# Kernel tuning notes

Hardware: AMD Instinct MI355X
Metric: run time of the kernel (lower is better)

## Reference

```python
import jax, jax.numpy as jnp
import numpy as np

N, E, C_IN, C_OUT, G = 100000, 1250000, 64, 64, 64
H = 2 * C_OUT  # hidden width of conv1 output


def _lin(k, out_d, in_d, scale=0.05):
    kw, kb = jax.random.split(k)
    return (jax.random.normal(kw, (out_d, in_d), jnp.float32) * scale,
            jax.random.normal(kb, (out_d,), jnp.float32) * scale)


def setup_inputs() -> dict:
    key = jax.random.key(0)
    ks = jax.random.split(key, 12)
    x = jax.random.normal(ks[0], (N, C_IN), jnp.float32)
    edge_index = jax.random.randint(ks[1], (2, E), 0, N, jnp.int64)
    batch = jnp.sort(jax.random.randint(ks[2], (N,), 0, G, jnp.int64))
    # GraphConv layer 1: lin_rel (with bias) on aggregated msgs, lin_root (no bias) on x
    w1_rel, b1_rel = _lin(ks[3], H, C_IN)
    w1_root = jax.random.normal(ks[4], (H, C_IN), jnp.float32) * 0.05
    # GraphConv layer 2
    w2_rel, b2_rel = _lin(ks[5], C_OUT, H)
    w2_root = jax.random.normal(ks[6], (C_OUT, H), jnp.float32) * 0.05
    # encoder_S: out_channels -> 8 -> 4 -> 1
    es_w1, es_b1 = _lin(ks[7], 8, C_OUT)
    es_w2, es_b2 = _lin(ks[8], 4, 8)
    es_w3, es_b3 = _lin(ks[9], 1, 4)
    # decoder: 1 -> 4 -> 8 -> out_channels (input dim fixed from buggy 2 to 1)
    d_w1, d_b1 = _lin(ks[10], 4, 1)
    d_w2, d_b2 = _lin(ks[11], 8, 4)
    d_w3, d_b3 = _lin(jax.random.fold_in(key, 99), C_OUT, 8)
    return dict(x=x, edge_index=edge_index, batch=batch,
                w1_rel=w1_rel, b1_rel=b1_rel, w1_root=w1_root,
                w2_rel=w2_rel, b2_rel=b2_rel, w2_root=w2_root,
                es_w1=es_w1, es_b1=es_b1, es_w2=es_w2, es_b2=es_b2,
                es_w3=es_w3, es_b3=es_b3,
                d_w1=d_w1, d_b1=d_b1, d_w2=d_w2, d_b2=d_b2,
                d_w3=d_w3, d_b3=d_b3)


def reference(x, edge_index, batch,
              w1_rel, b1_rel, w1_root,
              w2_rel, b2_rel, w2_root,
              es_w1, es_b1, es_w2, es_b2, es_w3, es_b3,
              d_w1, d_b1, d_w2, d_b2, d_w3, d_b3):
    src, dst = edge_index[0], edge_index[1]
    # GraphConv 1: sum-aggregate source feats into targets, then rel+root linears
    agg1 = jax.ops.segment_sum(x[src], dst, num_segments=N)  # [N, C_IN]
    h1 = jax.nn.relu(agg1 @ w1_rel.T + b1_rel + x @ w1_root.T)  # [N, H]
    # GraphConv 2
    agg2 = jax.ops.segment_sum(h1[src], dst, num_segments=N)
    h2 = jax.nn.relu(agg2 @ w2_rel.T + b2_rel + h1 @ w2_root.T)  # [N, C_OUT]
    # global mean pool over graphs
    counts = jax.ops.segment_sum(jnp.ones((N,), h2.dtype), batch, num_segments=G)
    h3 = jax.ops.segment_sum(h2, batch, num_segments=G) / jnp.maximum(counts, 1.0)[:, None]  # [G, C_OUT]
    # encoder_S MLP -> z
    z = jax.nn.relu(h3 @ es_w1.T + es_b1)
    z = jax.nn.relu(z @ es_w2.T + es_b2)
    z = z @ es_w3.T + es_b3  # [G, 1]
    # decoder MLP -> x_
    x_ = jax.nn.relu(z @ d_w1.T + d_b1)
    x_ = jax.nn.relu(x_ @ d_w2.T + d_b2)
    x_ = x_ @ d_w3.T + d_b3  # [G, C_OUT]
    return h3, x_
```

## Files before the change

### kernel.cpp

```cpp
#include <hip/hip_runtime.h>
#include <stdint.h>

#define NN 100000
#define EE 1250000
#define NBUCK 196
#define CHUNK 4096
#define NCHUNK ((EE + CHUNK - 1) / CHUNK)
#define PSLICE 24
#define XB_NB ((NN * 64 / 4 + 255) / 256)

typedef __attribute__((ext_vector_type(8))) short short8;
typedef __attribute__((ext_vector_type(4))) float f32x4;

__device__ inline ushort f2bf(float f) {
  union { float f; uint32_t u; } v; v.f = f;
  uint32_t r = v.u + 0x7FFF + ((v.u >> 16) & 1);
  return (ushort)(r >> 16);
}
__device__ inline float bf2f(ushort h) {
  union { uint32_t u; float f; } v; v.u = ((uint32_t)h) << 16;
  return v.f;
}

__global__ __launch_bounds__(256) void kfront(const float* __restrict__ w1_rel,
                                              const float* __restrict__ w1_root,
                                              const float* __restrict__ w2_rel,
                                              const float* __restrict__ w2_root,
                                              const float* __restrict__ x,
                                              const int* __restrict__ dstI,
                                              ushort* __restrict__ WF,
                                              ushort* __restrict__ xb,
                                              int* __restrict__ histG) {
  __shared__ int h[NBUCK];
  int t = threadIdx.x;
  int blk = blockIdx.x;
  if (blk < 32) {
    int idx = blk * 256 + t;
    if (idx < 8192) {
      int j = idx & 7, l = (idx >> 3) & 63, ts = idx >> 9;
      {
        int s = ts & 1, tt = ts >> 1;
        int o = tt * 16 + (l & 15), k = s * 32 + (l >> 4) * 8 + j;
        WF[idx] = f2bf(w1_rel[o * 64 + k]);
        WF[8192 + idx] = f2bf(w1_root[o * 64 + k]);
      }
      {
        int s = ts & 3, tt = ts >> 2;
        int o = tt * 16 + (l & 15), k = s * 32 + (l >> 4) * 8 + j;
        WF[16384 + idx] = f2bf(w2_rel[o * 128 + k]);
        WF[24576 + idx] = f2bf(w2_root[o * 128 + k]);
      }
    }
  } else if (blk < 32 + XB_NB) {
    int i = ((blk - 32) * 256 + t) * 4;
    if (i < NN * 64) {
      float4 v = *reinterpret_cast<const float4*>(x + i);
      ushort o[4] = {f2bf(v.x), f2bf(v.y), f2bf(v.z), f2bf(v.w)};
      *reinterpret_cast<uint2*>(xb + i) = *reinterpret_cast<uint2*>(o);
    }
  } else {
    int c = blk - 32 - XB_NB;
    if (t < NBUCK) h[t] = 0;
    __syncthreads();
    int cb = c * CHUNK;
    int cc = EE - cb; if (cc > CHUNK) cc = CHUNK;
    for (int i = t; i < cc; i += 256) atomicAdd(&h[dstI[cb + i] >> 9], 1);
    __syncthreads();
    if (t < NBUCK) histG[c * NBUCK + t] = h[t];
  }
}

__global__ __launch_bounds__(512) void kscan2d(const int* __restrict__ histG,
                                               int* __restrict__ relG,
                                               int* __restrict__ bucketTotal) {
  __shared__ int sm[512];
  int b = blockIdx.x;
  int t = threadIdx.x;
  int v = (t < NCHUNK) ? histG[t * NBUCK + b] : 0;
  sm[t] = v;
  __syncthreads();
  for (int d = 1; d < 512; d <<= 1) {
    int u = (t >= d) ? sm[t - d] : 0;
    __syncthreads();
    sm[t] += u;
    __syncthreads();
  }
  if (t < NCHUNK) relG[t * NBUCK + b] = sm[t] - v;
  if (t == 511) bucketTotal[b] = sm[511];
}

__global__ __launch_bounds__(256) void kbinA2(const int* __restrict__ srcI,
                                              const int* __restrict__ dstI,
                                              const int* __restrict__ histG,
                                              const int* __restrict__ relG,
                                              const int* __restrict__ bucketTotal,
                                              uint32_t* __restrict__ pairsG) {
  __shared__ uint32_t pko[CHUNK];
  __shared__ int ss[256];
  __shared__ int bsL[NBUCK];
  __shared__ int ex[NBUCK + 1];
  __shared__ int cur[NBUCK];
  __shared__ int gb[NBUCK];
  int t = threadIdx.x;
  int cb = blockIdx.x * CHUNK;
  int cc = EE - cb; if (cc > CHUNK) cc = CHUNK;

  {
    int bv = (t < NBUCK) ? bucketTotal[t] : 0;
    ss[t] = bv;
    __syncthreads();
    for (int d = 1; d < 256; d <<= 1) {
      int u = (t >= d) ? ss[t - d] : 0;
      __syncthreads();
      ss[t] += u;
      __syncthreads();
    }
    if (t < NBUCK) bsL[t] = ss[t] - bv;
    __syncthreads();
  }
  int v = (t < NBUCK) ? histG[blockIdx.x * NBUCK + t] : 0;
  ss[t] = v;
  __syncthreads();
  for (int d = 1; d < 256; d <<= 1) {
    int u = (t >= d) ? ss[t - d] : 0;
    __syncthreads();
    ss[t] += u;
    __syncthreads();
  }
  if (t < NBUCK) {
    ex[t] = ss[t] - v;
    cur[t] = ss[t] - v;
    gb[t] = bsL[t] + relG[blockIdx.x * NBUCK + t];
  }
  if (t == NBUCK - 1) ex[NBUCK] = ss[t];
  __syncthreads();
  for (int i = t; i < cc; i += 256) {
    int d = dstI[cb + i];
    int s = srcI[cb + i];
    int b = d >> 9;
    int p = atomicAdd(&cur[b], 1);
    pko[p] = (uint32_t)s | ((uint32_t)(d & 511) << 17);
  }
  __syncthreads();
  if (t < NBUCK) {
    int base = ex[t], cnt = ex[t + 1] - base, g0 = gb[t];
    for (int j = 0; j < cnt; ++j) pairsG[g0 + j] = pko[base + j];
  }
}

__global__ __launch_bounds__(256) void kbinB(const uint32_t* __restrict__ pairsG,
                                             const int* __restrict__ bucketTotal,
                                             int* __restrict__ starts,
                                             int* __restrict__ esrc) {
  __shared__ int hist[512];
  __shared__ int ex2[512];
  __shared__ int part[256];
  __shared__ int baseS;
  int t = threadIdx.x;
  int b = blockIdx.x;
  int nbase = b << 9;
  {
    int bv = (t < NBUCK) ? bucketTotal[t] : 0;
    part[t] = bv;
    __syncthreads();
    for (int d = 1; d < 256; d <<= 1) {
      int u = (t >= d) ? part[t - d] : 0;
      __syncthreads();
      part[t] += u;
      __syncthreads();
    }
    if (t == b) baseS = part[t] - bv;
    __syncthreads();
  }
  int base = baseS;
  int ecnt = bucketTotal[b];

  hist[t] = 0; hist[t + 256] = 0;
  __syncthreads();
  for (int i = t; i < ecnt; i += 256) atomicAdd(&hist[pairsG[base + i] >> 17], 1);
  __syncthreads();
  int a = hist[2 * t], c = hist[2 * t + 1];
  part[t] = a + c;
  __syncthreads();
  for (int d = 1; d < 256; d <<= 1) {
    int u = (t >= d) ? part[t - d] : 0;
    __syncthreads();
    part[t] += u;
    __syncthreads();
  }
  int pex = part[t] - (a + c);
  ex2[2 * t] = pex;
  ex2[2 * t + 1] = pex + a;
  __syncthreads();
  for (int n = t; n < 512; n += 256) {
    int node = nbase + n;
    if (node < NN) starts[node] = base + ex2[n];
  }
  if (b == NBUCK - 1 && t == 0) starts[NN] = EE;
  for (int n = t; n < 512; n += 256) hist[n] = ex2[n];
  __syncthreads();
  for (int i = t; i < ecnt; i += 256) {
    uint32_t p = pairsG[base + i];
    int dl = p >> 17;
    int s = p & 0x1FFFF;
    int lp = atomicAdd(&hist[dl], 1);
    esrc[base + lp] = s;
  }
}

#define ACC8(u)                                                                    \
  a0 += bf2f((ushort)(u).x); a1 += bf2f((ushort)((u).x >> 16));                    \
  a2 += bf2f((ushort)(u).y); a3 += bf2f((ushort)((u).y >> 16));                    \
  a4 += bf2f((ushort)(u).z); a5 += bf2f((ushort)((u).z >> 16));                    \
  a6 += bf2f((ushort)(u).w); a7 += bf2f((ushort)((u).w >> 16));

#define GATHER_CORE8(featb)                                                        \
  float a0 = 0.f, a1 = 0.f, a2 = 0.f, a3 = 0.f,                                    \
        a4 = 0.f, a5 = 0.f, a6 = 0.f, a7 = 0.f;                                    \
  const ushort* fb = (featb) + 8 * lg;                                             \
  int i = b;                                                                       \
  {                                                                                \
    int s0 = 0, s1 = 0, s2 = 0, s3 = 0, s4 = 0, s5 = 0, s6 = 0, s7 = 0;            \
    bool have = (i + 8 <= e);                                                      \
    if (have) {                                                                    \
      s0 = esrc[i];     s1 = esrc[i + 1]; s2 = esrc[i + 2]; s3 = esrc[i + 3];      \
      s4 = esrc[i + 4]; s5 = esrc[i + 5]; s6 = esrc[i + 6]; s7 = esrc[i + 7];      \
    }                                                                              \
    while (have) {                                                                 \
      uint4 u0 = *(const uint4*)(fb + (size_t)s0 * 64);                            \
      uint4 u1 = *(const uint4*)(fb + (size_t)s1 * 64);                            \
      uint4 u2 = *(const uint4*)(fb + (size_t)s2 * 64);                            \
      uint4 u3 = *(const uint4*)(fb + (size_t)s3 * 64);                            \
      uint4 u4 = *(const uint4*)(fb + (size_t)s4 * 64);                            \
      uint4 u5 = *(const uint4*)(fb + (size_t)s5 * 64);                            \
      uint4 u6 = *(const uint4*)(fb + (size_t)s6 * 64);                            \
      uint4 u7 = *(const uint4*)(fb + (size_t)s7 * 64);                            \
      i += 8;                                                                      \
      have = (i + 8 <= e);                                                         \
      if (have) {                                                                  \
        s0 = esrc[i];     s1 = esrc[i + 1]; s2 = esrc[i + 2]; s3 = esrc[i + 3];    \
        s4 = esrc[i + 4]; s5 = esrc[i + 5]; s6 = esrc[i + 6]; s7 = esrc[i + 7];    \
      }                                                                            \
      ACC8(u0) ACC8(u1) ACC8(u2) ACC8(u3) ACC8(u4) ACC8(u5) ACC8(u6) ACC8(u7)      \
    }                                                                              \
  }                                                                                \
  if (i + 4 <= e) {                                                                \
    int s0 = esrc[i], s1 = esrc[i + 1], s2 = esrc[i + 2], s3 = esrc[i + 3];        \
    uint4 u0 = *(const uint4*)(fb + (size_t)s0 * 64);                              \
    uint4 u1 = *(const uint4*)(fb + (size_t)s1 * 64);                              \
    uint4 u2 = *(const uint4*)(fb + (size_t)s2 * 64);                              \
    uint4 u3 = *(const uint4*)(fb + (size_t)s3 * 64);                              \
    ACC8(u0) ACC8(u1) ACC8(u2) ACC8(u3)                                            \
    i += 4;                                                                        \
  }                                                                                \
  if (i + 2 <= e) {                                                                \
    int s0 = esrc[i], s1 = esrc[i + 1];                                            \
    uint4 u0 = *(const uint4*)(fb + (size_t)s0 * 64);                              \
    uint4 u1 = *(const uint4*)(fb + (size_t)s1 * 64);                              \
    ACC8(u0) ACC8(u1)                                                              \
    i += 2;                                                                        \
  }                                                                                \
  if (i < e) {                                                                     \
    int s0 = esrc[i];                                                              \
    uint4 u0 = *(const uint4*)(fb + (size_t)s0 * 64);                              \
    ACC8(u0)                                                                       \
  }

__global__ __launch_bounds__(256) void kgatherQ(const ushort* __restrict__ featb,
                                                const int* __restrict__ starts,
                                                const int* __restrict__ esrc,
                                                ushort* __restrict__ outb) {
  int w = (blockIdx.x * 256 + threadIdx.x) >> 3;
  if (w >= NN) return;
  int lg = threadIdx.x & 7;
  int b = starts[w], e = starts[w + 1];
  GATHER_CORE8(featb)
  uint4 o;
  o.x = (uint32_t)f2bf(a0) | ((uint32_t)f2bf(a1) << 16);
  o.y = (uint32_t)f2bf(a2) | ((uint32_t)f2bf(a3) << 16);
  o.z = (uint32_t)f2bf(a4) | ((uint32_t)f2bf(a5) << 16);
  o.w = (uint32_t)f2bf(a6) | ((uint32_t)f2bf(a7) << 16);
  *(uint4*)(outb + (size_t)w * 64 + 8 * lg) = o;
}

__global__ __launch_bounds__(256) void kgh2Q(const ushort* __restrict__ featb,
                                             const int* __restrict__ starts,
                                             const int* __restrict__ esrc,
                                             const ushort* __restrict__ r2b,
                                             const float* __restrict__ b2v,
                                             ushort* __restrict__ h2b) {
  int w = (blockIdx.x * 256 + threadIdx.x) >> 3;
  if (w >= NN) return;
  int lg = threadIdx.x & 7;
  int b = starts[w], e = starts[w + 1];
  GATHER_CORE8(featb)
  uint4 ru = *(const uint4*)(r2b + (size_t)w * 64 + 8 * lg);
  float4 bA = *(const float4*)(b2v + 8 * lg);
  float4 bB = *(const float4*)(b2v + 8 * lg + 4);
  float v0 = fmaxf(a0 + bf2f((ushort)ru.x) + bA.x, 0.f);
  float v1 = fmaxf(a1 + bf2f((ushort)(ru.x >> 16)) + bA.y, 0.f);
  float v2 = fmaxf(a2 + bf2f((ushort)ru.y) + bA.z, 0.f);
  float v3 = fmaxf(a3 + bf2f((ushort)(ru.y >> 16)) + bA.w, 0.f);
  float v4 = fmaxf(a4 + bf2f((ushort)ru.z) + bB.x, 0.f);
  float v5 = fmaxf(a5 + bf2f((ushort)(ru.z >> 16)) + bB.y, 0.f);
  float v6 = fmaxf(a6 + bf2f((ushort)ru.w) + bB.z, 0.f);
  float v7 = fmaxf(a7 + bf2f((ushort)(ru.w >> 16)) + bB.w, 0.f);
  uint4 o;
  o.x = (uint32_t)f2bf(v0) | ((uint32_t)f2bf(v1) << 16);
  o.y = (uint32_t)f2bf(v2) | ((uint32_t)f2bf(v3) << 16);
  o.z = (uint32_t)f2bf(v4) | ((uint32_t)f2bf(v5) << 16);
  o.w = (uint32_t)f2bf(v6) | ((uint32_t)f2bf(v7) << 16);
  *(uint4*)(h2b + (size_t)w * 64 + 8 * lg) = o;
}

__global__ __launch_bounds__(256) void kfused(const ushort* __restrict__ xb,
                                              const ushort* __restrict__ aggb,
                                              const ushort* __restrict__ WF,
                                              const float* __restrict__ b1,
                                              ushort* __restrict__ y,
                                              ushort* __restrict__ r2b) {
  __shared__ __align__(16) char hT[32768];
  int t = threadIdx.x, l = t & 63, wv = t >> 6;
  int n0 = blockIdx.x * 128 + wv * 32;
  int row = l & 15;
  int kg = l >> 4;
  int nr0 = n0 + row;      if (nr0 > NN - 1) nr0 = NN - 1;
  int nr1 = n0 + 16 + row; if (nr1 > NN - 1) nr1 = NN - 1;

  short8 aA0[2], aX0[2], aA1[2], aX1[2];
  {
    const ushort* ap0 = aggb + (size_t)nr0 * 64 + kg * 8;
    aA0[0] = *(const short8*)(ap0);
    aA0[1] = *(const short8*)(ap0 + 32);
    const ushort* xp0 = xb + (size_t)nr0 * 64 + kg * 8;
    aX0[0] = *(const short8*)(xp0);
    aX0[1] = *(const short8*)(xp0 + 32);
    const ushort* ap1 = aggb + (size_t)nr1 * 64 + kg * 8;
    aA1[0] = *(const short8*)(ap1);
    aA1[1] = *(const short8*)(ap1 + 32);
    const ushort* xp1 = xb + (size_t)nr1 * 64 + kg * 8;
    aX1[0] = *(const short8*)(xp1);
    aX1[1] = *(const short8*)(xp1 + 32);
  }

  const ushort* wf1rel = WF;
  const ushort* wf1root = WF + 8192;
  char* base0 = hT + wv * 8192;
  char* base1 = base0 + 4096;

#pragma unroll
  for (int tt = 0; tt < 8; ++tt) {
    f32x4 acc0 = {0.f, 0.f, 0.f, 0.f};
    f32x4 acc1 = {0.f, 0.f, 0.f, 0.f};
#pragma unroll
    for (int s = 0; s < 2; ++s) {
      short8 br = *(const short8*)(wf1rel + ((size_t)(tt * 2 + s) * 64 + l) * 8);
      short8 bo = *(const short8*)(wf1root + ((size_t)(tt * 2 + s) * 64 + l) * 8);
      acc0 = __builtin_amdgcn_mfma_f32_16x16x32_bf16(aA0[s], br, acc0, 0, 0, 0);
      acc0 = __builtin_amdgcn_mfma_f32_16x16x32_bf16(aX0[s], bo, acc0, 0, 0, 0);
      acc1 = __builtin_amdgcn_mfma_f32_16x16x32_bf16(aA1[s], br, acc1, 0, 0, 0);
      acc1 = __builtin_amdgcn_mfma_f32_16x16x32_bf16(aX1[s], bo, acc1, 0, 0, 0);
    }
    float bias = b1[tt * 16 + row];
#pragma unroll
    for (int r = 0; r < 4; ++r) {
      int nl = kg * 4 + r;
      int off = nl * 256 + (tt * 16 + row) * 2;
      off ^= (nl & 7) << 4;
      *(ushort*)(base0 + off) = f2bf(fmaxf(acc0[r] + bias, 0.f));
      *(ushort*)(base1 + off) = f2bf(fmaxf(acc1[r] + bias, 0.f));
    }
  }
  __syncthreads();

  short8 aH0[4], aH1[4];
#pragma unroll
  for (int s = 0; s < 4; ++s) {
    int off = row * 256 + s * 64 + kg * 16;
    off ^= (row & 7) << 4;
    aH0[s] = *(const short8*)(base0 + off);
    aH1[s] = *(const short8*)(base1 + off);
  }

  const ushort* wf2rel = WF + 16384;
  const ushort* wf2root = WF + 24576;
#pragma unroll
  for (int tt = 0; tt < 4; ++tt) {
    f32x4 accY0 = {0.f, 0.f, 0.f, 0.f};
    f32x4 accR0 = {0.f, 0.f, 0.f, 0.f};
    f32x4 accY1 = {0.f, 0.f, 0.f, 0.f};
    f32x4 accR1 = {0.f, 0.f, 0.f, 0.f};
#pragma unroll
    for (int s = 0; s < 4; ++s) {
      short8 br = *(const short8*)(wf2rel + ((size_t)(tt * 4 + s) * 64 + l) * 8);
      short8 bo = *(const short8*)(wf2root + ((size_t)(tt * 4 + s) * 64 + l) * 8);
      accY0 = __builtin_amdgcn_mfma_f32_16x16x32_bf16(aH0[s], br, accY0, 0, 0, 0);
      accR0 = __builtin_amdgcn_mfma_f32_16x16x32_bf16(aH0[s], bo, accR0, 0, 0, 0);
      accY1 = __builtin_amdgcn_mfma_f32_16x16x32_bf16(aH1[s], br, accY1, 0, 0, 0);
      accR1 = __builtin_amdgcn_mfma_f32_16x16x32_bf16(aH1[s], bo, accR1, 0, 0, 0);
    }
#pragma unroll
    for (int r = 0; r < 4; ++r) {
      int nd0 = n0 + kg * 4 + r;
      int nd1 = nd0 + 16;
      if (nd0 < NN) {
        y[(size_t)nd0 * 64 + tt * 16 + row] = f2bf(accY0[r]);
        r2b[(size_t)nd0 * 64 + tt * 16 + row] = f2bf(accR0[r]);
      }
      if (nd1 < NN) {
        y[(size_t)nd1 * 64 + tt * 16 + row] = f2bf(accY1[r]);
        r2b[(size_t)nd1 * 64 + tt * 16 + row] = f2bf(accR1[r]);
      }
    }
  }
}

__global__ __launch_bounds__(256) void kpoolpart(const ushort* __restrict__ h2b,
                                                 const int* __restrict__ batch,
                                                 float* __restrict__ poolP) {
  __shared__ int gbs[2];
  __shared__ float part[4][64];
  int g = blockIdx.x / PSLICE, sl = blockIdx.x % PSLICE;
  int t = threadIdx.x;
  if (t < 2) {
    int target = g + t;
    int lo = 0, hi = NN;
    while (lo < hi) { int m = (lo + hi) >> 1; if (batch[m] < target) lo = m + 1; else hi = m; }
    gbs[t] = lo;
  }
  __syncthreads();
  int n0 = gbs[0], len = gbs[1] - n0;
  int lo = n0 + (int)((long)len * sl / PSLICE);
  int hi = n0 + (int)((long)len * (sl + 1) / PSLICE);
  int ch = t & 63, sub = t >> 6;
  float acc = 0.f;
  int n = lo + sub;
  for (; n + 12 < hi; n += 16) {
    float v0 = bf2f(h2b[(size_t)n * 64 + ch]);
    float v1 = bf2f(h2b[(size_t)(n + 4) * 64 + ch]);
    float v2 = bf2f(h2b[(size_t)(n + 8) * 64 + ch]);
    float v3 = bf2f(h2b[(size_t)(n + 12) * 64 + ch]);
    acc += (v0 + v1) + (v2 + v3);
  }
  for (; n < hi; n += 4) acc += bf2f(h2b[(size_t)n * 64 + ch]);
  part[sub][ch] = acc;
  __syncthreads();
  if (t < 64)
    poolP[(size_t)blockIdx.x * 64 + t] = part[0][t] + part[1][t] + part[2][t] + part[3][t];
}

__global__ __launch_bounds__(64) void kfinal3(
    const float* __restrict__ poolP, const int* __restrict__ batch,
    const float* __restrict__ es_w1, const float* __restrict__ es_b1,
    const float* __restrict__ es_w2, const float* __restrict__ es_b2,
    const float* __restrict__ es_w3, const float* __restrict__ es_b3,
    const float* __restrict__ d_w1, const float* __restrict__ d_b1,
    const float* __restrict__ d_w2, const float* __restrict__ d_b2,
    const float* __restrict__ d_w3, const float* __restrict__ d_b3,
    float* __restrict__ out) {
  __shared__ float h3[64];
  __shared__ float z1s[8];
  __shared__ float t2s[8];
  __shared__ int gbs[2];
  int g = blockIdx.x;
  int l = threadIdx.x;
  if (l < 2) {
    int target = g + l;
    int lo = 0, hi = NN;
    while (lo < hi) { int m = (lo + hi) >> 1; if (batch[m] < target) lo = m + 1; else hi = m; }
    gbs[l] = lo;
  }
  float s = 0.f;
#pragma unroll
  for (int k = 0; k < PSLICE; ++k) s += poolP[(size_t)(g * PSLICE + k) * 64 + l];
  __syncthreads();
  float c = fmaxf((float)(gbs[1] - gbs[0]), 1.f);
  float h = s / c;
  h3[l] = h;
  out[g * 64 + l] = h;
  __syncthreads();
  if (l < 8) {
    float a = es_b1[l];
#pragma unroll
    for (int k = 0; k < 64; ++k) a += es_w1[l * 64 + k] * h3[k];
    z1s[l] = fmaxf(a, 0.f);
  }
  __syncthreads();
  if (l == 0) {
    float z2[4];
#pragma unroll
    for (int j = 0; j < 4; ++j) {
      float a = es_b2[j];
#pragma unroll
      for (int k = 0; k < 8; ++k) a += es_w2[j * 8 + k] * z1s[k];
      z2[j] = fmaxf(a, 0.f);
    }
    float z = es_b3[0];
#pragma unroll
    for (int k = 0; k < 4; ++k) z += es_w3[k] * z2[k];
    float t1[4];
#pragma unroll
    for (int j = 0; j < 4; ++j) t1[j] = fmaxf(d_w1[j] * z + d_b1[j], 0.f);
#pragma unroll
    for (int j = 0; j < 8; ++j) {
      float a = d_b2[j];
#pragma unroll
      for (int k = 0; k < 4; ++k) a += d_w2[j * 4 + k] * t1[k];
      t2s[j] = fmaxf(a, 0.f);
    }
  }
  __syncthreads();
  float a = d_b3[l];
#pragma unroll
  for (int k = 0; k < 8; ++k) a += d_w3[l * 8 + k] * t2s[k];
  out[4096 + g * 64 + l] = a;
}

extern "C" void kernel_launch(void* const* d_in, const int* in_sizes, int n_in,
                              void* d_out, int out_size, void* d_ws, size_t ws_size,
                              hipStream_t stream) {
  const float* x = (const float*)d_in[0];
  const int* ei = (const int*)d_in[1];
  const int* srcI = ei;
  const int* dstI = ei + EE;
  const int* batch = (const int*)d_in[2];
  const float* w1_rel = (const float*)d_in[3];
  const float* b1_rel = (const float*)d_in[4];
  const float* w1_root = (const float*)d_in[5];
  const float* w2_rel = (const float*)d_in[6];
  const float* b2_rel = (const float*)d_in[7];
  const float* w2_root = (const float*)d_in[8];
  const float* es_w1 = (const float*)d_in[9];
  const float* es_b1 = (const float*)d_in[10];
  const float* es_w2 = (const float*)d_in[11];
  const float* es_b2 = (const float*)d_in[12];
  const float* es_w3 = (const float*)d_in[13];
  const float* es_b3 = (const float*)d_in[14];
  const float* d_w1 = (const float*)d_in[15];
  const float* d_b1 = (const float*)d_in[16];
  const float* d_w2 = (const float*)d_in[17];
  const float* d_b2 = (const float*)d_in[18];
  const float* d_w3 = (const float*)d_in[19];
  const float* d_b3 = (const float*)d_in[20];

  ushort* xb = (ushort*)d_ws;
  ushort* aggb = xb + (size_t)NN * 64;
  ushort* yb = aggb + (size_t)NN * 64;
  ushort* r2b = yb + (size_t)NN * 64;
  ushort* h2b = r2b + (size_t)NN * 64;
  ushort* WF = h2b + (size_t)NN * 64;
  float* poolP = (float*)(WF + 32768);
  int* starts = (int*)(poolP + 64 * PSLICE * 64);
  int* histG = starts + NN + 1;
  int* relG = histG + NCHUNK * NBUCK;
  int* bucketTotal = relG + NCHUNK * NBUCK;
  uint32_t* pairsG = (uint32_t*)(bucketTotal + NBUCK);
  int* esrc = (int*)(pairsG + EE);
  float* out = (float*)d_out;

  kfront<<<32 + XB_NB + NCHUNK, 256, 0, stream>>>(w1_rel, w1_root, w2_rel, w2_root,
                                                  x, dstI, WF, xb, histG);
  kscan2d<<<NBUCK, 512, 0, stream>>>(histG, relG, bucketTotal);
  kbinA2<<<NCHUNK, 256, 0, stream>>>(srcI, dstI, histG, relG, bucketTotal, pairsG);
  kbinB<<<NBUCK, 256, 0, stream>>>(pairsG, bucketTotal, starts, esrc);
  kgatherQ<<<(NN * 8 + 255) / 256, 256, 0, stream>>>(xb, starts, esrc, aggb);
  kfused<<<(NN + 127) / 128, 256, 0, stream>>>(xb, aggb, WF, b1_rel, yb, r2b);
  kgh2Q<<<(NN * 8 + 255) / 256, 256, 0, stream>>>(yb, starts, esrc, r2b, b2_rel, h2b);
  kpoolpart<<<64 * PSLICE, 256, 0, stream>>>(h2b, batch, poolP);
  kfinal3<<<64, 64, 0, stream>>>(poolP, batch, es_w1, es_b1, es_w2, es_b2, es_w3, es_b3,
                                 d_w1, d_b1, d_w2, d_b2, d_w3, d_b3, out);
}
```

Measured before the change: 135.3 us.

## Fuse layer-1 neighbor gather into MFMA linear kernel via shared memory

Merges the first sparse gather kernel into the fused MFMA linear kernel. Each block gathers aggregated features for its 128 nodes into swizzled LDS and feeds them straight to the MFMA stage. This removes one launch and the global write and read of the aggregated buffer. In exchange, LDS per block grows by 16KB, which lowers occupancy for the latency-bound gather phase, and the matrix work must wait behind a block-wide barrier.

```diff
diff --git a/kernel.cpp b/kernel.cpp
--- a/kernel.cpp
+++ b/kernel.cpp
@@ -215,8 +215,6 @@
   a6 += bf2f((ushort)(u).w); a7 += bf2f((ushort)((u).w >> 16));
 
 #define GATHER_CORE8(featb)                                                        \
-  float a0 = 0.f, a1 = 0.f, a2 = 0.f, a3 = 0.f,                                    \
-        a4 = 0.f, a5 = 0.f, a6 = 0.f, a7 = 0.f;                                    \
   const ushort* fb = (featb) + 8 * lg;                                             \
   int i = b;                                                                       \
   {                                                                                \
@@ -266,21 +264,136 @@
     ACC8(u0)                                                                       \
   }
 
-__global__ __launch_bounds__(256) void kgatherQ(const ushort* __restrict__ featb,
-                                                const int* __restrict__ starts,
-                                                const int* __restrict__ esrc,
-                                                ushort* __restrict__ outb) {
-  int w = (blockIdx.x * 256 + threadIdx.x) >> 3;
-  if (w >= NN) return;
-  int lg = threadIdx.x & 7;
-  int b = starts[w], e = starts[w + 1];
-  GATHER_CORE8(featb)
-  uint4 o;
-  o.x = (uint32_t)f2bf(a0) | ((uint32_t)f2bf(a1) << 16);
-  o.y = (uint32_t)f2bf(a2) | ((uint32_t)f2bf(a3) << 16);
-  o.z = (uint32_t)f2bf(a4) | ((uint32_t)f2bf(a5) << 16);
-  o.w = (uint32_t)f2bf(a6) | ((uint32_t)f2bf(a7) << 16);
-  *(uint4*)(outb + (size_t)w * 64 + 8 * lg) = o;
+__global__ __launch_bounds__(256) void kfusedG(const ushort* __restrict__ xb,
+                                               const int* __restrict__ starts,
+                                               const int* __restrict__ esrc,
+                                               const ushort* __restrict__ WF,
+                                               const float* __restrict__ b1,
+                                               ushort* __restrict__ y,
+                                               ushort* __restrict__ r2b) {
+  __shared__ __align__(16) char hT[32768];
+  __shared__ __align__(16) char aggL[16384];
+  int t = threadIdx.x, l = t & 63, wv = t >> 6;
+  int n0 = blockIdx.x * 128 + wv * 32;
+  int row = l & 15;
+  int kg = l >> 4;
+
+  {
+    int grp = t >> 3;
+    int lg = t & 7;
+#pragma unroll
+    for (int pass = 0; pass < 4; ++pass) {
+      int nl = pass * 32 + grp;
+      int w = blockIdx.x * 128 + nl;
+      float a0 = 0.f, a1 = 0.f, a2 = 0.f, a3 = 0.f,
+            a4 = 0.f, a5 = 0.f, a6 = 0.f, a7 = 0.f;
+      if (w < NN) {
+        int b = starts[w], e = starts[w + 1];
+        GATHER_CORE8(xb)
+      }
+      uint4 o;
+      o.x = (uint32_t)f2bf(a0) | ((uint32_t)f2bf(a1) << 16);
+      o.y = (uint32_t)f2bf(a2) | ((uint32_t)f2bf(a3) << 16);
+      o.z = (uint32_t)f2bf(a4) | ((uint32_t)f2bf(a5) << 16);
+      o.w = (uint32_t)f2bf(a6) | ((uint32_t)f2bf(a7) << 16);
+      int off = nl * 128 + lg * 16;
+      off ^= (nl & 7) << 4;
+      *(uint4*)(aggL + off) = o;
+    }
+  }
+  __syncthreads();
+
+  int nr0 = n0 + row;      if (nr0 > NN - 1) nr0 = NN - 1;
+  int nr1 = n0 + 16 + row; if (nr1 > NN - 1) nr1 = NN - 1;
+  int nl0 = wv * 32 + row, nl1 = nl0 + 16;
+
+  short8 aA0[2], aX0[2], aA1[2], aX1[2];
+  {
+#pragma unroll
+    for (int s = 0; s < 2; ++s) {
+      int off0 = nl0 * 128 + s * 64 + kg * 16; off0 ^= (nl0 & 7) << 4;
+      int off1 = nl1 * 128 + s * 64 + kg * 16; off1 ^= (nl1 & 7) << 4;
+      aA0[s] = *(const short8*)(aggL + off0);
+      aA1[s] = *(const short8*)(aggL + off1);
+    }
+    const ushort* xp0 = xb + (size_t)nr0 * 64 + kg * 8;
+    aX0[0] = *(const short8*)(xp0);
+    aX0[1] = *(const short8*)(xp0 + 32);
+    const ushort* xp1 = xb + (size_t)nr1 * 64 + kg * 8;
+    aX1[0] = *(const short8*)(xp1);
+    aX1[1] = *(const short8*)(xp1 + 32);
+  }
+
+  const ushort* wf1rel = WF;
+  const ushort* wf1root = WF + 8192;
+  char* base0 = hT + wv * 8192;
+  char* base1 = base0 + 4096;
+
+#pragma unroll
+  for (int tt = 0; tt < 8; ++tt) {
+    f32x4 acc0 = {0.f, 0.f, 0.f, 0.f};
+    f32x4 acc1 = {0.f, 0.f, 0.f, 0.f};
+#pragma unroll
+    for (int s = 0; s < 2; ++s) {
+      short8 br = *(const short8*)(wf1rel + ((size_t)(tt * 2 + s) * 64 + l) * 8);
+      short8 bo = *(const short8*)(wf1root + ((size_t)(tt * 2 + s) * 64 + l) * 8);
+      acc0 = __builtin_amdgcn_mfma_f32_16x16x32_bf16(aA0[s], br, acc0, 0, 0, 0);
+      acc0 = __builtin_amdgcn_mfma_f32_16x16x32_bf16(aX0[s], bo, acc0, 0, 0, 0);
+      acc1 = __builtin_amdgcn_mfma_f32_16x16x32_bf16(aA1[s], br, acc1, 0, 0, 0);
+      acc1 = __builtin_amdgcn_mfma_f32_16x16x32_bf16(aX1[s], bo, acc1, 0, 0, 0);
+    }
+    float bias = b1[tt * 16 + row];
+#pragma unroll
+    for (int r = 0; r < 4; ++r) {
+      int nl = kg * 4 + r;
+      int off = nl * 256 + (tt * 16 + row) * 2;
+      off ^= (nl & 7) << 4;
+      *(ushort*)(base0 + off) = f2bf(fmaxf(acc0[r] + bias, 0.f));
+      *(ushort*)(base1 + off) = f2bf(fmaxf(acc1[r] + bias, 0.f));
+    }
+  }
+  __syncthreads();
+
+  short8 aH0[4], aH1[4];
+#pragma unroll
+  for (int s = 0; s < 4; ++s) {
+    int off = row * 256 + s * 64 + kg * 16;
+    off ^= (row & 7) << 4;
+    aH0[s] = *(const short8*)(base0 + off);
+    aH1[s] = *(const short8*)(base1 + off);
+  }
+
+  const ushort* wf2rel = WF + 16384;
+  const ushort* wf2root = WF + 24576;
+#pragma unroll
+  for (int tt = 0; tt < 4; ++tt) {
+    f32x4 accY0 = {0.f, 0.f, 0.f, 0.f};
+    f32x4 accR0 = {0.f, 0.f, 0.f, 0.f};
+    f32x4 accY1 = {0.f, 0.f, 0.f, 0.f};
+    f32x4 accR1 = {0.f, 0.f, 0.f, 0.f};
+#pragma unroll
+    for (int s = 0; s < 4; ++s) {
+      short8 br = *(const short8*)(wf2rel + ((size_t)(tt * 4 + s) * 64 + l) * 8);
+      short8 bo = *(const short8*)(wf2root + ((size_t)(tt * 4 + s) * 64 + l) * 8);
+      accY0 = __builtin_amdgcn_mfma_f32_16x16x32_bf16(aH0[s], br, accY0, 0, 0, 0);
+      accR0 = __builtin_amdgcn_mfma_f32_16x16x32_bf16(aH0[s], bo, accR0, 0, 0, 0);
+      accY1 = __builtin_amdgcn_mfma_f32_16x16x32_bf16(aH1[s], br, accY1, 0, 0, 0);
+      accR1 = __builtin_amdgcn_mfma_f32_16x16x32_bf16(aH1[s], bo, accR1, 0, 0, 0);
+    }
+#pragma unroll
+    for (int r = 0; r < 4; ++r) {
+      int nd0 = n0 + kg * 4 + r;
+      int nd1 = nd0 + 16;
+      if (nd0 < NN) {
+        y[(size_t)nd0 * 64 + tt * 16 + row] = f2bf(accY0[r]);
+        r2b[(size_t)nd0 * 64 + tt * 16 + row] = f2bf(accR0[r]);
+      }
+      if (nd1 < NN) {
+        y[(size_t)nd1 * 64 + tt * 16 + row] = f2bf(accY1[r]);
+        r2b[(size_t)nd1 * 64 + tt * 16 + row] = f2bf(accR1[r]);
+      }
+    }
+  }
 }
 
 __global__ __launch_bounds__(256) void kgh2Q(const ushort* __restrict__ featb,
@@ -293,6 +406,8 @@
   if (w >= NN) return;
   int lg = threadIdx.x & 7;
   int b = starts[w], e = starts[w + 1];
+  float a0 = 0.f, a1 = 0.f, a2 = 0.f, a3 = 0.f,
+        a4 = 0.f, a5 = 0.f, a6 = 0.f, a7 = 0.f;
   GATHER_CORE8(featb)
   uint4 ru = *(const uint4*)(r2b + (size_t)w * 64 + 8 * lg);
   float4 bA = *(const float4*)(b2v + 8 * lg);
@@ -311,108 +426,6 @@
   o.z = (uint32_t)f2bf(v4) | ((uint32_t)f2bf(v5) << 16);
   o.w = (uint32_t)f2bf(v6) | ((uint32_t)f2bf(v7) << 16);
   *(uint4*)(h2b + (size_t)w * 64 + 8 * lg) = o;
-}
-
-__global__ __launch_bounds__(256) void kfused(const ushort* __restrict__ xb,
-                                              const ushort* __restrict__ aggb,
-                                              const ushort* __restrict__ WF,
-                                              const float* __restrict__ b1,
-                                              ushort* __restrict__ y,
-                                              ushort* __restrict__ r2b) {
-  __shared__ __align__(16) char hT[32768];
-  int t = threadIdx.x, l = t & 63, wv = t >> 6;
-  int n0 = blockIdx.x * 128 + wv * 32;
-  int row = l & 15;
-  int kg = l >> 4;
-  int nr0 = n0 + row;      if (nr0 > NN - 1) nr0 = NN - 1;
-  int nr1 = n0 + 16 + row; if (nr1 > NN - 1) nr1 = NN - 1;
-
-  short8 aA0[2], aX0[2], aA1[2], aX1[2];
-  {
-    const ushort* ap0 = aggb + (size_t)nr0 * 64 + kg * 8;
-    aA0[0] = *(const short8*)(ap0);
-    aA0[1] = *(const short8*)(ap0 + 32);
-    const ushort* xp0 = xb + (size_t)nr0 * 64 + kg * 8;
-    aX0[0] = *(const short8*)(xp0);
-    aX0[1] = *(const short8*)(xp0 + 32);
-    const ushort* ap1 = aggb + (size_t)nr1 * 64 + kg * 8;
-    aA1[0] = *(const short8*)(ap1);
-    aA1[1] = *(const short8*)(ap1 + 32);
-    const ushort* xp1 = xb + (size_t)nr1 * 64 + kg * 8;
-    aX1[0] = *(const short8*)(xp1);
-    aX1[1] = *(const short8*)(xp1 + 32);
-  }
-
-  const ushort* wf1rel = WF;
-  const ushort* wf1root = WF + 8192;
-  char* base0 = hT + wv * 8192;
-  char* base1 = base0 + 4096;
-
-#pragma unroll
-  for (int tt = 0; tt < 8; ++tt) {
-    f32x4 acc0 = {0.f, 0.f, 0.f, 0.f};
-    f32x4 acc1 = {0.f, 0.f, 0.f, 0.f};
-#pragma unroll
-    for (int s = 0; s < 2; ++s) {
-      short8 br = *(const short8*)(wf1rel + ((size_t)(tt * 2 + s) * 64 + l) * 8);
-      short8 bo = *(const short8*)(wf1root + ((size_t)(tt * 2 + s) * 64 + l) * 8);
-      acc0 = __builtin_amdgcn_mfma_f32_16x16x32_bf16(aA0[s], br, acc0, 0, 0, 0);
-      acc0 = __builtin_amdgcn_mfma_f32_16x16x32_bf16(aX0[s], bo, acc0, 0, 0, 0);
-      acc1 = __builtin_amdgcn_mfma_f32_16x16x32_bf16(aA1[s], br, acc1, 0, 0, 0);
-      acc1 = __builtin_amdgcn_mfma_f32_16x16x32_bf16(aX1[s], bo, acc1, 0, 0, 0);
-    }
-    float bias = b1[tt * 16 + row];
-#pragma unroll
-    for (int r = 0; r < 4; ++r) {
-      int nl = kg * 4 + r;
-      int off = nl * 256 + (tt * 16 + row) * 2;
-      off ^= (nl & 7) << 4;
-      *(ushort*)(base0 + off) = f2bf(fmaxf(acc0[r] + bias, 0.f));
-      *(ushort*)(base1 + off) = f2bf(fmaxf(acc1[r] + bias, 0.f));
-    }
-  }
-  __syncthreads();
-
-  short8 aH0[4], aH1[4];
-#pragma unroll
-  for (int s = 0; s < 4; ++s) {
-    int off = row * 256 + s * 64 + kg * 16;
-    off ^= (row & 7) << 4;
-    aH0[s] = *(const short8*)(base0 + off);
-    aH1[s] = *(const short8*)(base1 + off);
-  }
-
-  const ushort* wf2rel = WF + 16384;
-  const ushort* wf2root = WF + 24576;
-#pragma unroll
-  for (int tt = 0; tt < 4; ++tt) {
-    f32x4 accY0 = {0.f, 0.f, 0.f, 0.f};
-    f32x4 accR0 = {0.f, 0.f, 0.f, 0.f};
-    f32x4 accY1 = {0.f, 0.f, 0.f, 0.f};
-    f32x4 accR1 = {0.f, 0.f, 0.f, 0.f};
-#pragma unroll
-    for (int s = 0; s < 4; ++s) {
-      short8 br = *(const short8*)(wf2rel + ((size_t)(tt * 4 + s) * 64 + l) * 8);
-      short8 bo = *(const short8*)(wf2root + ((size_t)(tt * 4 + s) * 64 + l) * 8);
-      accY0 = __builtin_amdgcn_mfma_f32_16x16x32_bf16(aH0[s], br, accY0, 0, 0, 0);
-      accR0 = __builtin_amdgcn_mfma_f32_16x16x32_bf16(aH0[s], bo, accR0, 0, 0, 0);
-      accY1 = __builtin_amdgcn_mfma_f32_16x16x32_bf16(aH1[s], br, accY1, 0, 0, 0);
-      accR1 = __builtin_amdgcn_mfma_f32_16x16x32_bf16(aH1[s], bo, accR1, 0, 0, 0);
-    }
-#pragma unroll
-    for (int r = 0; r < 4; ++r) {
-      int nd0 = n0 + kg * 4 + r;
-      int nd1 = nd0 + 16;
-      if (nd0 < NN) {
-        y[(size_t)nd0 * 64 + tt * 16 + row] = f2bf(accY0[r]);
-        r2b[(size_t)nd0 * 64 + tt * 16 + row] = f2bf(accR0[r]);
-      }
-      if (nd1 < NN) {
-        y[(size_t)nd1 * 64 + tt * 16 + row] = f2bf(accY1[r]);
-        r2b[(size_t)nd1 * 64 + tt * 16 + row] = f2bf(accR1[r]);
-      }
-    }
-  }
 }
 
 __global__ __launch_bounds__(256) void kpoolpart(const ushort* __restrict__ h2b,
@@ -544,8 +557,7 @@
   const float* d_b3 = (const float*)d_in[20];
 
   ushort* xb = (ushort*)d_ws;
-  ushort* aggb = xb + (size_t)NN * 64;
-  ushort* yb = aggb + (size_t)NN * 64;
+  ushort* yb = xb + (size_t)NN * 64;
   ushort* r2b = yb + (size_t)NN * 64;
   ushort* h2b = r2b + (size_t)NN * 64;
   ushort* WF = h2b + (size_t)NN * 64;
@@ -563,8 +575,7 @@
   kscan2d<<<NBUCK, 512, 0, stream>>>(histG, relG, bucketTotal);
   kbinA2<<<NCHUNK, 256, 0, stream>>>(srcI, dstI, histG, relG, bucketTotal, pairsG);
   kbinB<<<NBUCK, 256, 0, stream>>>(pairsG, bucketTotal, starts, esrc);
-  kgatherQ<<<(NN * 8 + 255) / 256, 256, 0, stream>>>(xb, starts, esrc, aggb);
-  kfused<<<(NN + 127) / 128, 256, 0, stream>>>(xb, aggb, WF, b1_rel, yb, r2b);
+  kfusedG<<<(NN + 127) / 128, 256, 0, stream>>>(xb, starts, esrc, WF, b1_rel, yb, r2b);
   kgh2Q<<<(NN * 8 + 255) / 256, 256, 0, stream>>>(yb, starts, esrc, r2b, b2_rel, h2b);
   kpoolpart<<<64 * PSLICE, 256, 0, stream>>>(h2b, batch, poolP);
   kfinal3<<<64, 64, 0, stream>>>(poolP, batch, es_w1, es_b1, es_w2, es_b2, es_w3, es_b3,
```

Result: slower. 145.2 us (+7.3%).
